# Kernel tuning notes

Measured on AMD Instinct MI355X. Metric: run time of the kernel, lower is better.

The kernel has to match this reference:

```python
import jax, jax.numpy as jnp
import numpy as np

# Dims from LiftSplatShootGPN defaults
B, N, D, FH, FW, C = 8, 6, 41, 8, 22, 64
OGFH, OGFW = 128, 352
DX = jnp.array([0.5, 0.5, 20.0], dtype=jnp.float32)        # gen_dx_bx
BX = jnp.array([-49.75, -49.75, 0.0], dtype=jnp.float32)
NX = (200, 200, 1)


def _frustum():
    # D x fH x fW x 3, matches create_frustum
    ds = jnp.broadcast_to(jnp.arange(4.0, 45.0, 1.0, dtype=jnp.float32).reshape(D, 1, 1), (D, FH, FW))
    xs = jnp.broadcast_to(jnp.linspace(0.0, OGFW - 1.0, FW, dtype=jnp.float32).reshape(1, 1, FW), (D, FH, FW))
    ys = jnp.broadcast_to(jnp.linspace(0.0, OGFH - 1.0, FH, dtype=jnp.float32).reshape(1, FH, 1), (D, FH, FW))
    return jnp.stack((xs, ys, ds), -1)


def setup_inputs() -> dict:
    key = jax.random.key(0)
    k1, k2, k3, k4, k5, k6 = jax.random.split(key, 6)
    eye = jnp.eye(3, dtype=jnp.float32)
    x_feats = jax.random.normal(k1, (B, N, D, FH, FW, C), dtype=jnp.float32)
    # well-conditioned camera extrinsics / intrinsics
    rots = eye + 0.1 * jax.random.normal(k2, (B, N, 3, 3), dtype=jnp.float32)
    trans = 2.0 * jax.random.normal(k3, (B, N, 3), dtype=jnp.float32)
    intr_base = jnp.array([[278.0, 0.0, 176.0], [0.0, 278.0, 64.0], [0.0, 0.0, 1.0]], dtype=jnp.float32)
    intrins = intr_base + 0.5 * jax.random.normal(k4, (B, N, 3, 3), dtype=jnp.float32) * jnp.array([[1, 0, 1], [0, 1, 1], [0, 0, 0]], dtype=jnp.float32)
    post_rots = eye + 0.01 * jax.random.normal(k5, (B, N, 3, 3), dtype=jnp.float32)
    post_trans = 0.5 * jax.random.normal(k6, (B, N, 3), dtype=jnp.float32)
    return {"x_feats": x_feats, "rots": rots, "trans": trans, "intrins": intrins,
            "post_rots": post_rots, "post_trans": post_trans}


def _forward(x_feats, rots, trans, intrins, post_rots, post_trans):
    frustum = _frustum()  # [D,FH,FW,3]
    # get_geometry: undo image-space augmentation
    pts = frustum[None, None] - post_trans[:, :, None, None, None, :]            # [B,N,D,H,W,3]
    inv_pr = jnp.linalg.inv(post_rots)                                           # [B,N,3,3]
    pts = jnp.einsum('bnij,bndhwj->bndhwi', inv_pr, pts)
    # unproject: (u*d, v*d, d)
    pts = jnp.concatenate((pts[..., :2] * pts[..., 2:3], pts[..., 2:3]), axis=-1)
    combine = jnp.einsum('bnij,bnjk->bnik', rots, jnp.linalg.inv(intrins))
    geom = jnp.einsum('bnij,bndhwj->bndhwi', combine, pts) + trans[:, :, None, None, None, :]

    # voxel_pooling
    Nprime = B * N * D * FH * FW
    x = x_feats.reshape(Nprime, C)
    # torch .long() truncates toward zero -> astype(int32) matches
    g = ((geom - (BX - DX / 2.0)) / DX).reshape(Nprime, 3).astype(jnp.int32)
    bix = jnp.repeat(jnp.arange(B, dtype=jnp.int32), Nprime // B)
    kept = ((g[:, 0] >= 0) & (g[:, 0] < NX[0]) &
            (g[:, 1] >= 0) & (g[:, 1] < NX[1]) &
            (g[:, 2] >= 0) & (g[:, 2] < NX[2]))
    # QuickCumsum computes per-voxel segment sums; scatter-add of all kept points
    # into the dense grid yields identical values without the sort.
    flat = ((bix * NX[2] + g[:, 2]) * NX[0] + g[:, 0]) * NX[1] + g[:, 1]
    flat = jnp.where(kept, flat, 0)
    xm = jnp.where(kept[:, None], x, jnp.zeros((), x.dtype))
    grid = jnp.zeros((B * NX[2] * NX[0] * NX[1], C), dtype=x.dtype).at[flat].add(xm)
    # final: [B, C, nz, nx0, nx1] -> cat over nz (nz=1) -> [B, C, 200, 200]
    grid = grid.reshape(B, NX[2], NX[0], NX[1], C)
    final = jnp.transpose(grid, (0, 1, 4, 2, 3)).reshape(B, NX[2] * C, NX[0], NX[1])
    return final


def reference(x_feats, rots, trans, intrins, post_rots, post_trans):
    return _forward(x_feats, rots, trans, intrins, post_rots, post_trans)
```

## Files before the change

### kernel.cpp

```cpp
#include <hip/hip_runtime.h>

#define B_   8
#define N_   6
#define D_   41
#define FH_  8
#define FW_  22
#define C_   64
#define NPRIME (B_*N_*D_*FH_*FW_)
#define NBLK_PTS 1353
#define NX0  200
#define NX1  200
#define G1Q  4
#define NB2  (B_ * NX0 * G1Q)
#define OUTSZ (B_*C_*NX0*NX1)
#define CAP  512
#define DIRECT_N 16
#define MAXTASKS 8192

__device__ void lapack_inv3_f32(const float Ain[9], float Aout[9]) {
    #pragma clang fp contract(off)
    float a[9];
    for (int r = 0; r < 3; ++r)
        for (int c = 0; c < 3; ++c)
            a[c*3 + r] = Ain[r*3 + c];
    int ipiv[3];
    for (int j = 0; j < 3; ++j) {
        int p = j;
        float amax = fabsf(a[j*3 + j]);
        for (int i = j + 1; i < 3; ++i) {
            float v = fabsf(a[j*3 + i]);
            if (v > amax) { amax = v; p = i; }
        }
        ipiv[j] = p;
        if (p != j)
            for (int c = 0; c < 3; ++c) { float t = a[c*3+j]; a[c*3+j] = a[c*3+p]; a[c*3+p] = t; }
        float d = 1.0f / a[j*3 + j];
        for (int i = j + 1; i < 3; ++i) a[j*3 + i] = a[j*3 + i] * d;
        for (int jj = j + 1; jj < 3; ++jj) {
            float temp = -a[jj*3 + j];
            for (int ii = j + 1; ii < 3; ++ii)
                a[jj*3 + ii] = a[jj*3 + ii] + a[j*3 + ii] * temp;
        }
    }
    for (int j = 0; j < 3; ++j) {
        float ajj_inv = 1.0f / a[j*3 + j];
        a[j*3 + j] = ajj_inv;
        float AJJ = -ajj_inv;
        for (int jj = 0; jj < j; ++jj) {
            float temp = a[j*3 + jj];
            for (int i = 0; i < jj; ++i)
                a[j*3 + i] = a[j*3 + i] + temp * a[jj*3 + i];
            a[j*3 + jj] = a[j*3 + jj] * a[jj*3 + jj];
        }
        for (int i = 0; i < j; ++i) a[j*3 + i] = a[j*3 + i] * AJJ;
    }
    float work[3];
    for (int j = 2; j >= 0; --j) {
        for (int i = j + 1; i < 3; ++i) { work[i] = a[j*3 + i]; a[j*3 + i] = 0.0f; }
        for (int jj = j + 1; jj < 3; ++jj) {
            float temp = -work[jj];
            for (int i = 0; i < 3; ++i)
                a[j*3 + i] = a[j*3 + i] + temp * a[jj*3 + i];
        }
    }
    for (int j = 2; j >= 0; --j) {
        int p = ipiv[j];
        if (p != j)
            for (int i = 0; i < 3; ++i) { float t = a[j*3+i]; a[j*3+i] = a[p*3+i]; a[p*3+i] = t; }
    }
    for (int r = 0; r < 3; ++r)
        for (int c = 0; c < 3; ++c)
            Aout[r*3 + c] = a[c*3 + r];
}

__global__ void prep_kernel(const float* __restrict__ rots,
                            const float* __restrict__ trans,
                            const float* __restrict__ intrins,
                            const float* __restrict__ post_rots,
                            const float* __restrict__ post_trans,
                            float* __restrict__ mats,
                            int* __restrict__ counts,
                            int* __restrict__ task_count) {
    #pragma clang fp contract(off)
    int t = threadIdx.x;
    for (int i = t; i < NB2; i += 256) counts[i] = 0;
    if (t == 0) task_count[0] = 0;
    if (t >= B_ * N_) return;
    float pr[9], ipr[9], K[9], iK[9];
    for (int i = 0; i < 9; ++i) { pr[i] = post_rots[t*9 + i]; K[i] = intrins[t*9 + i]; }
    lapack_inv3_f32(pr, ipr);
    lapack_inv3_f32(K, iK);
    float* m = mats + t * 24;
    for (int i = 0; i < 9; ++i) m[i] = ipr[i];
    for (int i = 0; i < 3; ++i)
        for (int k = 0; k < 3; ++k) {
            float s = rots[t*9 + i*3 + 0] * iK[0*3 + k];
            s = s + rots[t*9 + i*3 + 1] * iK[1*3 + k];
            s = s + rots[t*9 + i*3 + 2] * iK[2*3 + k];
            m[9 + i*3 + k] = s;
        }
    for (int i = 0; i < 3; ++i) {
        m[18 + i] = post_trans[t*3 + i];
        m[21 + i] = trans[t*3 + i];
    }
}

__global__ void __launch_bounds__(256) geom_kernel(
        const float* __restrict__ mats,
        unsigned int* __restrict__ pcode,
        int* __restrict__ counts,
        float4* __restrict__ out4) {
    #pragma clang fp contract(off)
    __shared__ unsigned int hist[NB2];
    int t = threadIdx.x;
    int p = blockIdx.x * 256 + t;
    for (int i = t; i < NB2; i += 256) hist[i] = 0u;
    __syncthreads();

    int w  = p % FW_;
    int h  = (p / FW_) % FH_;
    int d  = (p / (FW_ * FH_)) % D_;
    int bn = p / (FW_ * FH_ * D_);
    int b  = bn / N_;

    const float* m = mats + bn * 24;

    float xs = (w == FW_ - 1) ? 351.0f : (float)((double)w * (351.0 / 21.0));
    float ys = (h == FH_ - 1) ? 127.0f : (float)((double)h * (127.0 / 7.0));
    float ds = 4.0f + (float)d;

    float px = xs - m[18], py = ys - m[19], pz = ds - m[20];
    float qx = m[0]*px;  qx = qx + m[1]*py;  qx = qx + m[2]*pz;
    float qy = m[3]*px;  qy = qy + m[4]*py;  qy = qy + m[5]*pz;
    float qz = m[6]*px;  qz = qz + m[7]*py;  qz = qz + m[8]*pz;

    float ux = qx * qz, uy = qy * qz, uz = qz;

    float gx = m[9]*ux;   gx = gx + m[10]*uy;  gx = gx + m[11]*uz;  gx = gx + m[21];
    float gy = m[12]*ux;  gy = gy + m[13]*uy;  gy = gy + m[14]*uz;  gy = gy + m[22];
    float gz = m[15]*ux;  gz = gz + m[16]*uy;  gz = gz + m[17]*uz;  gz = gz + m[23];

    float cx = (gx - (-50.0f)) / 0.5f;
    float cy = (gy - (-50.0f)) / 0.5f;
    float cz = (gz - (-10.0f)) / 20.0f;
    int g0 = (int)cx;
    int g1 = (int)cy;
    int g2 = (int)cz;

    bool kept = (g0 >= 0) && (g0 < NX0) && (g1 >= 0) && (g1 < NX1) && (g2 == 0);
    if (kept) {
        int g1q = g1 / 50;
        int g1r = g1 - g1q * 50;
        int bk  = (b * NX0 + g0) * G1Q + g1q;
        pcode[p] = ((unsigned int)bk << 6) | (unsigned int)g1r;
        atomicAdd(&hist[bk], 1u);
    } else {
        pcode[p] = 0xFFFFFFFFu;
    }
    __syncthreads();
    for (int i = t; i < NB2; i += 256) {
        unsigned int hv = hist[i];
        if (hv) atomicAdd(&counts[i], (int)hv);
    }

    const int TOT4 = OUTSZ / 4;
    float4 z4 = make_float4(0.f, 0.f, 0.f, 0.f);
    for (int i = p; i < TOT4; i += NPRIME) out4[i] = z4;
}

__global__ void scan_kernel(const int* __restrict__ counts,
                            int* __restrict__ offsets,
                            int* __restrict__ cursor,
                            unsigned int* __restrict__ tasks,
                            int* __restrict__ task_count) {
    __shared__ int ts[256];
    int t = threadIdx.x;
    const int PER = NB2 / 256;
    int base = t * PER;
    int mysum = 0;
    for (int j = 0; j < PER; ++j) mysum += counts[base + j];
    ts[t] = mysum;
    __syncthreads();
    for (int off = 1; off < 256; off <<= 1) {
        int v = (t >= off) ? ts[t - off] : 0;
        __syncthreads();
        ts[t] += v;
        __syncthreads();
    }
    int run = (t > 0) ? ts[t - 1] : 0;
    int ltasks = 0;
    for (int j = 0; j < PER; ++j) {
        int c = counts[base + j];
        offsets[base + j] = run;
        cursor[base + j]  = run;
        run += c;
        if (c > 0) ltasks += (c + CAP - 1) / CAP;
    }
    if (t == 255) offsets[NB2] = run;
    int tpos = (ltasks > 0) ? atomicAdd(task_count, ltasks) : 0;
    for (int j = 0; j < PER; ++j) {
        int c = counts[base + j];
        if (c <= 0) continue;
        int nch = (c + CAP - 1) / CAP;
        unsigned int sole = (nch == 1) ? (1u << 31) : 0u;
        for (int k = 0; k < nch; ++k)
            tasks[tpos++] = sole | ((unsigned int)(base + j) << 9) | (unsigned int)k;
    }
}

__global__ void __launch_bounds__(256) place_kernel(
        const unsigned int* __restrict__ pcode,
        int* __restrict__ cursor,
        unsigned int* __restrict__ entries) {
    __shared__ unsigned int cnt[NB2];
    __shared__ int gbase[NB2];
    int t = threadIdx.x;
    int p = blockIdx.x * 256 + t;
    for (int i = t; i < NB2; i += 256) cnt[i] = 0u;
    __syncthreads();
    unsigned int code = pcode[p];
    bool kept = (code != 0xFFFFFFFFu);
    int bk = (int)(code >> 6);
    unsigned int lr = 0;
    if (kept) lr = atomicAdd(&cnt[bk], 1u);
    __syncthreads();
    for (int i = t; i < NB2; i += 256) {
        unsigned int c = cnt[i];
        if (c) gbase[i] = atomicAdd(&cursor[i], (int)c);
    }
    __syncthreads();
    if (kept)
        entries[gbase[bk] + (int)lr] = ((code & 63u) << 19) | (unsigned int)p;
}

#define LDS_STRIDE 51
__global__ void __launch_bounds__(512) gather_kernel(
        const float* __restrict__ x_feats,
        const unsigned int* __restrict__ entries,
        const int* __restrict__ offsets,
        const unsigned int* __restrict__ tasks,
        const int* __restrict__ task_count,
        float* __restrict__ out) {
    __shared__ float acc[C_ * LDS_STRIDE];
    __shared__ unsigned int ecache[CAP];
    __shared__ int touched[50];
    int bid = blockIdx.x;
    if (bid >= task_count[0]) return;
    unsigned int task = tasks[bid];
    int sole = (int)(task >> 31);
    int bk   = (int)((task >> 9) & 0x1FFFu);
    int ch   = (int)(task & 0x1FFu);
    int s = offsets[bk] + ch * CAP;
    int e = offsets[bk + 1];
    if (e > s + CAP) e = s + CAP;
    int n = e - s;

    int t = threadIdx.x, wave = t >> 6, lane = t & 63;
    int b   = bk / (NX0 * G1Q);
    int rem = bk % (NX0 * G1Q);
    int g0  = rem / G1Q, g1q = rem % G1Q;
    size_t obase = (size_t)b * (C_ * NX0 * NX1) + (size_t)g0 * NX1 + g1q * 50;

    if (n <= DIRECT_N) {
        for (int i = wave; i < n; i += 8) {
            unsigned int v = entries[s + i];
            float f = x_feats[(size_t)(v & 0x7FFFFu) * C_ + lane];
            unsafeAtomicAdd(&out[obase + (size_t)lane * (NX0 * NX1) + (int)(v >> 19)], f);
        }
        return;
    }

    for (int i = t; i < C_ * LDS_STRIDE; i += 512) acc[i] = 0.0f;
    if (t < 50) touched[t] = 0;
    if (t < n) ecache[t] = entries[s + t];
    __syncthreads();

    int i = wave * 4;
    for (; i + 4 <= n; i += 32) {
        unsigned int v0 = ecache[i],     v1 = ecache[i + 1];
        unsigned int v2 = ecache[i + 2], v3 = ecache[i + 3];
        float f0 = x_feats[(size_t)(v0 & 0x7FFFFu) * C_ + lane];
        float f1 = x_feats[(size_t)(v1 & 0x7FFFFu) * C_ + lane];
        float f2 = x_feats[(size_t)(v2 & 0x7FFFFu) * C_ + lane];
        float f3 = x_feats[(size_t)(v3 & 0x7FFFFu) * C_ + lane];
        if (lane == 0) {
            touched[v0 >> 19] = 1; touched[v1 >> 19] = 1;
            touched[v2 >> 19] = 1; touched[v3 >> 19] = 1;
        }
        atomicAdd(&acc[lane * LDS_STRIDE + (int)(v0 >> 19)], f0);
        atomicAdd(&acc[lane * LDS_STRIDE + (int)(v1 >> 19)], f1);
        atomicAdd(&acc[lane * LDS_STRIDE + (int)(v2 >> 19)], f2);
        atomicAdd(&acc[lane * LDS_STRIDE + (int)(v3 >> 19)], f3);
    }
    for (; i < n; ++i) {
        unsigned int v = ecache[i];
        float f = x_feats[(size_t)(v & 0x7FFFFu) * C_ + lane];
        if (lane == 0) touched[v >> 19] = 1;
        atomicAdd(&acc[lane * LDS_STRIDE + (int)(v >> 19)], f);
    }
    __syncthreads();

    for (int k = t; k < C_ * 50; k += 512) {
        int c = k / 50, r = k - c * 50;
        if (!touched[r]) continue;
        float val = acc[c * LDS_STRIDE + r];
        if (val != 0.0f) {
            float* dst = &out[obase + (size_t)c * (NX0 * NX1) + r];
            if (sole) *dst = val;
            else unsafeAtomicAdd(dst, val);
        }
    }
}

extern "C" void kernel_launch(void* const* d_in, const int* in_sizes, int n_in,
                              void* d_out, int out_size, void* d_ws, size_t ws_size,
                              hipStream_t stream) {
    const float* x_feats    = (const float*)d_in[0];
    const float* rots       = (const float*)d_in[1];
    const float* trans      = (const float*)d_in[2];
    const float* intrins    = (const float*)d_in[3];
    const float* post_rots  = (const float*)d_in[4];
    const float* post_trans = (const float*)d_in[5];
    float* out = (float*)d_out;

    char* w = (char*)d_ws;
    float*        mats       = (float*)w;         w += 48 * 24 * sizeof(float);
    int*          counts     = (int*)w;           w += NB2 * sizeof(int);
    int*          offsets    = (int*)w;           w += (NB2 + 1) * sizeof(int);
    int*          cursor     = (int*)w;           w += NB2 * sizeof(int);
    int*          task_count = (int*)w;           w += 4 * sizeof(int);
    unsigned int* tasks      = (unsigned int*)w;  w += MAXTASKS * sizeof(unsigned int);
    unsigned int* pcode      = (unsigned int*)w;  w += NPRIME * sizeof(unsigned int);
    unsigned int* entries    = (unsigned int*)w;  w += NPRIME * sizeof(unsigned int);

    prep_kernel<<<1, 256, 0, stream>>>(rots, trans, intrins, post_rots, post_trans,
                                       mats, counts, task_count);
    geom_kernel<<<NBLK_PTS, 256, 0, stream>>>(mats, pcode, counts, (float4*)out);
    scan_kernel<<<1, 256, 0, stream>>>(counts, offsets, cursor, tasks, task_count);
    place_kernel<<<NBLK_PTS, 256, 0, stream>>>(pcode, cursor, entries);
    gather_kernel<<<MAXTASKS, 512, 0, stream>>>(x_feats, entries, offsets,
                                                tasks, task_count, out);
}
```

Before: 224.1 us.

## Use persistent gather blocks with atomic work queue and deterministic task ordering

Replaces the launch of one gather block per task (up to 8192 blocks of 512 threads) with 1024 persistent 256-thread blocks that pull tasks from a global atomic cursor. The scan now builds task offsets with a prefix sum instead of per-thread atomics, which keeps task order deterministic. Chunk size drops to 256 and the direct-atomic threshold rises to 48. The LDS entry cache and the touched-row tracking are removed, so every block now scans the full accumulator on writeback. The intent is to cut block-launch overhead and balance uneven bin sizes, at the cost of smaller blocks and extra per-task syncs.

```diff
diff --git a/kernel.cpp b/kernel.cpp
--- a/kernel.cpp
+++ b/kernel.cpp
@@ -13,9 +13,10 @@
 #define G1Q  4
 #define NB2  (B_ * NX0 * G1Q)
 #define OUTSZ (B_*C_*NX0*NX1)
-#define CAP  512
-#define DIRECT_N 16
+#define CAP  256
+#define DIRECT_N 48
 #define MAXTASKS 8192
+#define GATHER_BLOCKS 1024
 
 __device__ void lapack_inv3_f32(const float Ain[9], float Aout[9]) {
     #pragma clang fp contract(off)
@@ -79,12 +80,10 @@
                             const float* __restrict__ post_rots,
                             const float* __restrict__ post_trans,
                             float* __restrict__ mats,
-                            int* __restrict__ counts,
-                            int* __restrict__ task_count) {
+                            int* __restrict__ counts) {
     #pragma clang fp contract(off)
     int t = threadIdx.x;
     for (int i = t; i < NB2; i += 256) counts[i] = 0;
-    if (t == 0) task_count[0] = 0;
     if (t >= B_ * N_) return;
     float pr[9], ipr[9], K[9], iK[9];
     for (int i = 0; i < 9; ++i) { pr[i] = post_rots[t*9 + i]; K[i] = intrins[t*9 + i]; }
@@ -172,39 +171,48 @@
                             int* __restrict__ offsets,
                             int* __restrict__ cursor,
                             unsigned int* __restrict__ tasks,
-                            int* __restrict__ task_count) {
+                            int* __restrict__ task_count,
+                            int* __restrict__ wcursor) {
     __shared__ int ts[256];
+    __shared__ int tbase_s[256];
     int t = threadIdx.x;
     const int PER = NB2 / 256;
     int base = t * PER;
-    int mysum = 0;
-    for (int j = 0; j < PER; ++j) mysum += counts[base + j];
+    int mysum = 0, mytasks = 0;
+    for (int j = 0; j < PER; ++j) {
+        int c = counts[base + j];
+        mysum += c;
+        if (c > 0) mytasks += (c + CAP - 1) / CAP;
+    }
     ts[t] = mysum;
+    tbase_s[t] = mytasks;
     __syncthreads();
     for (int off = 1; off < 256; off <<= 1) {
-        int v = (t >= off) ? ts[t - off] : 0;
+        int v  = (t >= off) ? ts[t - off] : 0;
+        int tv = (t >= off) ? tbase_s[t - off] : 0;
         __syncthreads();
         ts[t] += v;
-        __syncthreads();
-    }
-    int run = (t > 0) ? ts[t - 1] : 0;
-    int ltasks = 0;
+        tbase_s[t] += tv;
+        __syncthreads();
+    }
+    int run  = (t > 0) ? ts[t - 1] : 0;
+    int tpos = (t > 0) ? tbase_s[t - 1] : 0;
     for (int j = 0; j < PER; ++j) {
         int c = counts[base + j];
         offsets[base + j] = run;
         cursor[base + j]  = run;
         run += c;
-        if (c > 0) ltasks += (c + CAP - 1) / CAP;
-    }
-    if (t == 255) offsets[NB2] = run;
-    int tpos = (ltasks > 0) ? atomicAdd(task_count, ltasks) : 0;
-    for (int j = 0; j < PER; ++j) {
-        int c = counts[base + j];
-        if (c <= 0) continue;
-        int nch = (c + CAP - 1) / CAP;
-        unsigned int sole = (nch == 1) ? (1u << 31) : 0u;
-        for (int k = 0; k < nch; ++k)
-            tasks[tpos++] = sole | ((unsigned int)(base + j) << 9) | (unsigned int)k;
+        if (c > 0) {
+            int nch = (c + CAP - 1) / CAP;
+            unsigned int sole = (nch == 1) ? (1u << 31) : 0u;
+            for (int k = 0; k < nch; ++k)
+                tasks[tpos++] = sole | ((unsigned int)(base + j) << 12) | (unsigned int)k;
+        }
+    }
+    if (t == 255) {
+        offsets[NB2] = run;
+        task_count[0] = tbase_s[255];
+        wcursor[0] = 0;
     }
 }
 
@@ -212,103 +220,103 @@
         const unsigned int* __restrict__ pcode,
         int* __restrict__ cursor,
         unsigned int* __restrict__ entries) {
-    __shared__ unsigned int cnt[NB2];
-    __shared__ int gbase[NB2];
+    __shared__ int cnt[NB2];
     int t = threadIdx.x;
     int p = blockIdx.x * 256 + t;
-    for (int i = t; i < NB2; i += 256) cnt[i] = 0u;
+    for (int i = t; i < NB2; i += 256) cnt[i] = 0;
     __syncthreads();
     unsigned int code = pcode[p];
     bool kept = (code != 0xFFFFFFFFu);
     int bk = (int)(code >> 6);
-    unsigned int lr = 0;
-    if (kept) lr = atomicAdd(&cnt[bk], 1u);
+    int lr = 0;
+    if (kept) lr = atomicAdd(&cnt[bk], 1);
     __syncthreads();
     for (int i = t; i < NB2; i += 256) {
-        unsigned int c = cnt[i];
-        if (c) gbase[i] = atomicAdd(&cursor[i], (int)c);
+        int c = cnt[i];
+        if (c) cnt[i] = atomicAdd(&cursor[i], c);
     }
     __syncthreads();
     if (kept)
-        entries[gbase[bk] + (int)lr] = ((code & 63u) << 19) | (unsigned int)p;
+        entries[cnt[bk] + lr] = ((code & 63u) << 19) | (unsigned int)p;
 }
 
 #define LDS_STRIDE 51
-__global__ void __launch_bounds__(512) gather_kernel(
+__global__ void __launch_bounds__(256) gather_kernel(
         const float* __restrict__ x_feats,
         const unsigned int* __restrict__ entries,
         const int* __restrict__ offsets,
         const unsigned int* __restrict__ tasks,
         const int* __restrict__ task_count,
+        int* __restrict__ wcursor,
         float* __restrict__ out) {
     __shared__ float acc[C_ * LDS_STRIDE];
-    __shared__ unsigned int ecache[CAP];
-    __shared__ int touched[50];
-    int bid = blockIdx.x;
-    if (bid >= task_count[0]) return;
-    unsigned int task = tasks[bid];
-    int sole = (int)(task >> 31);
-    int bk   = (int)((task >> 9) & 0x1FFFu);
-    int ch   = (int)(task & 0x1FFu);
-    int s = offsets[bk] + ch * CAP;
-    int e = offsets[bk + 1];
-    if (e > s + CAP) e = s + CAP;
-    int n = e - s;
-
+    __shared__ int sh_task;
+    int ntask = task_count[0];
     int t = threadIdx.x, wave = t >> 6, lane = t & 63;
-    int b   = bk / (NX0 * G1Q);
-    int rem = bk % (NX0 * G1Q);
-    int g0  = rem / G1Q, g1q = rem % G1Q;
-    size_t obase = (size_t)b * (C_ * NX0 * NX1) + (size_t)g0 * NX1 + g1q * 50;
-
-    if (n <= DIRECT_N) {
-        for (int i = wave; i < n; i += 8) {
+
+    for (;;) {
+        if (t == 0) sh_task = atomicAdd(wcursor, 1);
+        __syncthreads();
+        int tid = sh_task;
+        __syncthreads();
+        if (tid >= ntask) return;
+
+        unsigned int task = tasks[tid];
+        int sole = (int)(task >> 31);
+        int bk   = (int)((task >> 12) & 0x1FFFu);
+        int ch   = (int)(task & 0xFFFu);
+        int s = offsets[bk] + ch * CAP;
+        int e = offsets[bk + 1];
+        if (e > s + CAP) e = s + CAP;
+        int n = e - s;
+
+        int b   = bk / (NX0 * G1Q);
+        int rem = bk % (NX0 * G1Q);
+        int g0  = rem / G1Q, g1q = rem % G1Q;
+        size_t obase = (size_t)b * (C_ * NX0 * NX1) + (size_t)g0 * NX1 + g1q * 50;
+
+        if (n <= DIRECT_N) {
+            for (int i = wave; i < n; i += 4) {
+                unsigned int v = entries[s + i];
+                float f = x_feats[(size_t)(v & 0x7FFFFu) * C_ + lane];
+                unsafeAtomicAdd(&out[obase + (size_t)lane * (NX0 * NX1) + (int)(v >> 19)], f);
+            }
+            continue;
+        }
+
+        for (int i = t; i < C_ * LDS_STRIDE; i += 256) acc[i] = 0.0f;
+        __syncthreads();
+
+        int i = wave * 4;
+        for (; i + 4 <= n; i += 16) {
+            unsigned int v0 = entries[s + i],     v1 = entries[s + i + 1];
+            unsigned int v2 = entries[s + i + 2], v3 = entries[s + i + 3];
+            float f0 = x_feats[(size_t)(v0 & 0x7FFFFu) * C_ + lane];
+            float f1 = x_feats[(size_t)(v1 & 0x7FFFFu) * C_ + lane];
+            float f2 = x_feats[(size_t)(v2 & 0x7FFFFu) * C_ + lane];
+            float f3 = x_feats[(size_t)(v3 & 0x7FFFFu) * C_ + lane];
+            atomicAdd(&acc[lane * LDS_STRIDE + (int)(v0 >> 19)], f0);
+            atomicAdd(&acc[lane * LDS_STRIDE + (int)(v1 >> 19)], f1);
+            atomicAdd(&acc[lane * LDS_STRIDE + (int)(v2 >> 19)], f2);
+            atomicAdd(&acc[lane * LDS_STRIDE + (int)(v3 >> 19)], f3);
+        }
+        for (; i < n; ++i) {
             unsigned int v = entries[s + i];
             float f = x_feats[(size_t)(v & 0x7FFFFu) * C_ + lane];
-            unsafeAtomicAdd(&out[obase + (size_t)lane * (NX0 * NX1) + (int)(v >> 19)], f);
-        }
-        return;
-    }
-
-    for (int i = t; i < C_ * LDS_STRIDE; i += 512) acc[i] = 0.0f;
-    if (t < 50) touched[t] = 0;
-    if (t < n) ecache[t] = entries[s + t];
-    __syncthreads();
-
-    int i = wave * 4;
-    for (; i + 4 <= n; i += 32) {
-        unsigned int v0 = ecache[i],     v1 = ecache[i + 1];
-        unsigned int v2 = ecache[i + 2], v3 = ecache[i + 3];
-        float f0 = x_feats[(size_t)(v0 & 0x7FFFFu) * C_ + lane];
-        float f1 = x_feats[(size_t)(v1 & 0x7FFFFu) * C_ + lane];
-        float f2 = x_feats[(size_t)(v2 & 0x7FFFFu) * C_ + lane];
-        float f3 = x_feats[(size_t)(v3 & 0x7FFFFu) * C_ + lane];
-        if (lane == 0) {
-            touched[v0 >> 19] = 1; touched[v1 >> 19] = 1;
-            touched[v2 >> 19] = 1; touched[v3 >> 19] = 1;
-        }
-        atomicAdd(&acc[lane * LDS_STRIDE + (int)(v0 >> 19)], f0);
-        atomicAdd(&acc[lane * LDS_STRIDE + (int)(v1 >> 19)], f1);
-        atomicAdd(&acc[lane * LDS_STRIDE + (int)(v2 >> 19)], f2);
-        atomicAdd(&acc[lane * LDS_STRIDE + (int)(v3 >> 19)], f3);
-    }
-    for (; i < n; ++i) {
-        unsigned int v = ecache[i];
-        float f = x_feats[(size_t)(v & 0x7FFFFu) * C_ + lane];
-        if (lane == 0) touched[v >> 19] = 1;
-        atomicAdd(&acc[lane * LDS_STRIDE + (int)(v >> 19)], f);
-    }
-    __syncthreads();
-
-    for (int k = t; k < C_ * 50; k += 512) {
-        int c = k / 50, r = k - c * 50;
-        if (!touched[r]) continue;
-        float val = acc[c * LDS_STRIDE + r];
-        if (val != 0.0f) {
-            float* dst = &out[obase + (size_t)c * (NX0 * NX1) + r];
-            if (sole) *dst = val;
-            else unsafeAtomicAdd(dst, val);
-        }
+            atomicAdd(&acc[lane * LDS_STRIDE + (int)(v >> 19)], f);
+        }
+        __syncthreads();
+
+        for (int k = t; k < C_ * 50; k += 256) {
+            int c = k / 50, r = k - c * 50;
+            float val = acc[c * LDS_STRIDE + r];
+            if (val != 0.0f) {
+                float* dst = &out[obase + (size_t)c * (NX0 * NX1) + r];
+                if (sole) *dst = val;
+                else unsafeAtomicAdd(dst, val);
+            }
+        }
+        __syncthreads();
     }
 }
 
@@ -329,15 +337,17 @@
     int*          offsets    = (int*)w;           w += (NB2 + 1) * sizeof(int);
     int*          cursor     = (int*)w;           w += NB2 * sizeof(int);
     int*          task_count = (int*)w;           w += 4 * sizeof(int);
+    int*          wcursor    = (int*)w;           w += 4 * sizeof(int);
     unsigned int* tasks      = (unsigned int*)w;  w += MAXTASKS * sizeof(unsigned int);
     unsigned int* pcode      = (unsigned int*)w;  w += NPRIME * sizeof(unsigned int);
     unsigned int* entries    = (unsigned int*)w;  w += NPRIME * sizeof(unsigned int);
 
     prep_kernel<<<1, 256, 0, stream>>>(rots, trans, intrins, post_rots, post_trans,
-                                       mats, counts, task_count);
+                                       mats, counts);
     geom_kernel<<<NBLK_PTS, 256, 0, stream>>>(mats, pcode, counts, (float4*)out);
-    scan_kernel<<<1, 256, 0, stream>>>(counts, offsets, cursor, tasks, task_count);
+    scan_kernel<<<1, 256, 0, stream>>>(counts, offsets, cursor, tasks,
+                                       task_count, wcursor);
     place_kernel<<<NBLK_PTS, 256, 0, stream>>>(pcode, cursor, entries);
-    gather_kernel<<<MAXTASKS, 512, 0, stream>>>(x_feats, entries, offsets,
-                                                tasks, task_count, out);
-}
+    gather_kernel<<<GATHER_BLOCKS, 256, 0, stream>>>(x_feats, entries, offsets,
+                                                     tasks, task_count, wcursor, out);
+}
```

Result: slower. 235.9 us (+5.2%).
